# Kernel tuning notes

Hardware: AMD Instinct MI355X
Metric: run time of the kernel (lower is better)

## Reference

```python
import jax, jax.numpy as jnp
import numpy as np

B, T, C, H = 1, 1024, 2048, 32
N = C // H  # head_dim = 64
EPS_GN = 0.00064


def setup_inputs() -> dict:
    key = jax.random.key(0)
    ks = jax.random.split(key, 40)
    f32 = jnp.float32

    def rn(k, shape, s):
        return jax.random.normal(k, shape, f32) * s

    layer_idx, n_layer = 12, 24
    r01 = layer_idx / (n_layer - 1)
    r1a0 = 1.0 - layer_idx / n_layer
    ddd = (jnp.arange(C, dtype=f32) / C).reshape(1, 1, C)
    decay_speed = -7.0 + 5.0 * (jnp.arange(C, dtype=f32) / (C - 1)) ** (0.85 + r01 ** 0.5)

    inp = dict(
        hidden_states=jax.random.normal(ks[0], (B, T, C), f32),
        Wq=rn(ks[1], (C, C), 0.02), Wk=rn(ks[2], (C, C), 0.02),
        Wv=rn(ks[3], (C, C), 0.02), Wo=rn(ks[4], (C, C), 0.02),
        time_maa_x=1.0 - ddd ** (0.6 * r1a0 ** 0.9),
        time_maa_rg=rn(ks[5], (1, 1, C), 0.01),
        time_maa_wa=rn(ks[6], (1, 1, C), 0.01),
        time_maa_k=rn(ks[7], (1, 1, C), 0.01),
        time_maa_v=rn(ks[8], (1, 1, C), 0.01),
        time_maa_w1=rn(ks[9], (C, 4 * 32), 0.01),
        time_maa_w2=rn(ks[10], (4, 32, C), 0.01),
        time_decay=decay_speed.reshape(1, 1, C) + 0.5,
        time_decay_w1=rn(ks[11], (C, 64), 0.01),
        time_decay_w2=rn(ks[12], (64, C), 0.01),
        time_aaaaa=rn(ks[13], (1, 1, C), 0.01),
        time_aaa_w1=rn(ks[14], (C, 16), 0.01),
        time_aaa_w2=rn(ks[15], (16, C), 0.01),
        time_kkk_w1=rn(ks[16], (C, 16), 0.01),
        time_kkk_w2=rn(ks[17], (16, C), 0.01),
        gate_w1=rn(ks[18], (C, 128), 0.01),
        gate_w2=rn(ks[19], (128, C), 0.01),
        time_misc_a=rn(ks[20], (1, 1, C), 0.01),
        ma_w1=rn(ks[21], (C, 16), 0.01),
        ma_w2=rn(ks[22], (16, C), 0.01),
        time_misc_k=rn(ks[23], (1, 1, C), 0.01),
        mk_w1=rn(ks[24], (C, 16), 0.01),
        mk_w2=rn(ks[25], (16, C), 0.01),
        time_faaaa=rn(ks[26], (1, 1, H, N), 0.01),
        ln_w=1.0 + rn(ks[27], (C,), 0.01),
        ln_b=rn(ks[28], (C,), 0.01),
    )
    return inp


def _wkv7(r, w, k, v, a, b):
    """RWKV7 matrix-state recurrence. Inputs [B,T,C]; per head state [N,N].
    state_t = state * exp(w_t) (per key-col) + (state @ a_t) b_t^T + v_t k_t^T;
    out_t = state_t @ r_t."""
    hs = lambda x: x.reshape(B, T, H, N)
    r, k, v, a, b = map(hs, (r, k, v, a, b))
    dec = jnp.exp(hs(w))  # w <= -0.5, decay in (0,1)

    def step(state, inp):
        r_t, d_t, k_t, v_t, a_t, b_t = inp  # each [B,H,N]
        sa = jnp.einsum('bhij,bhj->bhi', state, a_t)
        state = (state * d_t[:, :, None, :]
                 + sa[..., None] * b_t[:, :, None, :]
                 + v_t[..., None] * k_t[:, :, None, :])
        out = jnp.einsum('bhij,bhj->bhi', state, r_t)
        return state, out

    xs = tuple(jnp.moveaxis(t, 1, 0) for t in (r, dec, k, v, a, b))  # [T,B,H,N]
    state0 = jnp.zeros((B, H, N, N), r.dtype)
    _, out = jax.lax.scan(step, state0, xs)
    return jnp.moveaxis(out, 0, 1).reshape(B, T, C)


def _group_norm(x, w, b):
    xg = x.reshape(B, T, H, N)
    mu = xg.mean(-1, keepdims=True)
    var = xg.var(-1, keepdims=True)
    xn = (xg - mu) * jax.lax.rsqrt(var + EPS_GN)
    return xn.reshape(B, T, C) * w + b


def reference(hidden_states, Wq, Wk, Wv, Wo, time_maa_x, time_maa_rg, time_maa_wa,
              time_maa_k, time_maa_v, time_maa_w1, time_maa_w2, time_decay,
              time_decay_w1, time_decay_w2, time_aaaaa, time_aaa_w1, time_aaa_w2,
              time_kkk_w1, time_kkk_w2, gate_w1, gate_w2, time_misc_a, ma_w1, ma_w2,
              time_misc_k, mk_w1, mk_w2, time_faaaa, ln_w, ln_b):
    x = hidden_states  # T already multiple of 16, so no padding branch
    dxprev = jnp.pad(x, ((0, 0), (1, 0), (0, 0)))[:, :-1] - x  # token shift
    xxx = x + dxprev * time_maa_x
    mix = jnp.tanh(xxx @ time_maa_w1).reshape(B, T, 4, 32)
    mix = jnp.einsum('btfd,fdc->fbtc', mix, time_maa_w2)  # [4,B,T,C]
    mrg, mwa, mk_mix, mv = mix[0], mix[1], mix[2], mix[3]
    xrg = x + dxprev * (time_maa_rg + mrg)
    xwa = x + dxprev * (time_maa_wa + mwa)
    xk = x + dxprev * (time_maa_k + mk_mix)
    xv = x + dxprev * (time_maa_v + mv)

    r = xrg @ Wq
    w = -jax.nn.softplus(-(time_decay + jnp.tanh(xwa @ time_decay_w1) @ time_decay_w2)) - 0.5
    k = xk @ Wk
    v = xv @ Wv
    g = jnp.tanh(xrg @ gate_w1) @ gate_w2

    kk = k + jnp.tanh(xk @ time_kkk_w1) @ time_kkk_w2
    kkh = kk.reshape(B, T, H, N)
    kk = (kkh / jnp.maximum(jnp.linalg.norm(kkh, axis=-1, keepdims=True), 1e-12)).reshape(B, T, C)

    a = jax.nn.sigmoid(time_aaaaa + (xwa @ time_aaa_w1) @ time_aaa_w2)
    ma = jax.nn.sigmoid(time_misc_a + (xwa @ ma_w1) @ ma_w2)
    k = k * ma + k * a * (1.0 - ma)
    mk_g = jax.nn.sigmoid(time_misc_k + (xk @ mk_w1) @ mk_w2)
    k = k * jnp.exp(jnp.minimum(w * mk_g, 0.0))

    y = _wkv7(r, w, k, v, -kk, kk * a)
    y = _group_norm(y, ln_w, ln_b)
    rh, kh, vh = (t.reshape(B, T, H, N) for t in (r, k, v))
    y = y + ((rh * kh * time_faaaa).sum(-1, keepdims=True) * vh).reshape(B, T, C)
    return (y * g) @ Wo
```

## Files before the change

### kernel.cpp

```cpp
#include <hip/hip_runtime.h>


#define T_ 1024
#define C_ 2048
#define H_ 32
#define N_ 64

using half8  = __attribute__((ext_vector_type(8))) _Float16;
using half4  = __attribute__((ext_vector_type(4))) _Float16;
using floatx4 = __attribute__((ext_vector_type(4))) float;

#define DPP_ADD(v, ctrl) \
    ((v) + __int_as_float(__builtin_amdgcn_update_dpp( \
        0, __float_as_int(v), (ctrl), 0xf, 0xf, true)))
#define REDUCE16(v) do { \
    v = DPP_ADD(v, 0xB1); v = DPP_ADD(v, 0x4E); \
    v = DPP_ADD(v, 0x141); v = DPP_ADD(v, 0x140); } while (0)

__device__ __forceinline__ void async_cp16(const void* g, void* l) {
    __builtin_amdgcn_global_load_lds(
        (const __attribute__((address_space(1))) void*)g,
        (__attribute__((address_space(3))) void*)l, 16, 0, 0);
}

__global__ __launch_bounds__(256) void k_tr(
    const float* __restrict__ W0, const float* __restrict__ W1,
    const float* __restrict__ W2, const float* __restrict__ W3,
    _Float16* __restrict__ D0, _Float16* __restrict__ D1,
    _Float16* __restrict__ D2, _Float16* __restrict__ D3)
{
    const int z = blockIdx.z;
    const float* S = (z == 0) ? W0 : (z == 1) ? W1 : (z == 2) ? W2 : W3;
    _Float16* D = (z == 0) ? D0 : (z == 1) ? D1 : (z == 2) ? D2 : D3;
    const int nb = blockIdx.x * 64, kb = blockIdx.y * 64;
    __shared__ __align__(16) float tile[64][65];
    const int tr = threadIdx.x >> 4, tc4 = (threadIdx.x & 15) * 4;
#pragma unroll
    for (int p = 0; p < 4; ++p) {
        int row = p * 16 + tr;
        float4 v = *(const float4*)&S[(size_t)(kb + row) * C_ + nb + tc4];
        tile[row][tc4 + 0] = v.x; tile[row][tc4 + 1] = v.y;
        tile[row][tc4 + 2] = v.z; tile[row][tc4 + 3] = v.w;
    }
    __syncthreads();
#pragma unroll
    for (int p = 0; p < 4; ++p) {
        int n = p * 16 + tr;
        half4 u;
        u[0] = (_Float16)tile[tc4 + 0][n];
        u[1] = (_Float16)tile[tc4 + 1][n];
        u[2] = (_Float16)tile[tc4 + 2][n];
        u[3] = (_Float16)tile[tc4 + 3][n];
        *(half4*)&D[(size_t)(nb + n) * C_ + kb + tc4] = u;
    }
}

__global__ __launch_bounds__(256) void k_trW(
    const float* __restrict__ maa_w1, const float* __restrict__ gate_w1,
    const float* __restrict__ decay_w1, const float* __restrict__ aaa_w1,
    const float* __restrict__ ma_w1, const float* __restrict__ kkk_w1,
    const float* __restrict__ mk_w1,
    _Float16* __restrict__ WTm, _Float16* __restrict__ WTl)
{
    const int z = blockIdx.z;
    const int k = blockIdx.x * 256 + threadIdx.x;
    const int n = blockIdx.y;
    if (z == 0 && n >= 128) return;
    const float* src; int stride, col;
    _Float16* dst;
    if (z == 0) { src = maa_w1; stride = 128; col = n; dst = WTm; }
    else {
        dst = WTl;
        if (n < 128)      { src = gate_w1;  stride = 128; col = n; }
        else if (n < 192) { src = decay_w1; stride = 64;  col = n - 128; }
        else if (n < 208) { src = aaa_w1;   stride = 16;  col = n - 192; }
        else if (n < 224) { src = ma_w1;    stride = 16;  col = n - 208; }
        else if (n < 240) { src = kkk_w1;   stride = 16;  col = n - 224; }
        else              { src = mk_w1;    stride = 16;  col = n - 240; }
    }
    dst[(size_t)n * C_ + k] = (_Float16)src[(size_t)k * stride + col];
}

__global__ __launch_bounds__(256) void k_prep(
    const float* __restrict__ X, const float* __restrict__ maa_x,
    _Float16* __restrict__ xxxH)
{
    const size_t idx = (size_t)blockIdx.x * 256 + threadIdx.x;
    const int c = (int)(idx & (C_ - 1));
    float cur = X[idx];
    float prev = (idx >= C_) ? X[idx - C_] : 0.0f;
    xxxH[idx] = (_Float16)(cur + (prev - cur) * maa_x[c]);
}

__global__ __launch_bounds__(256) void k_lora(
    int which,
    const _Float16* __restrict__ Axxx, const _Float16* __restrict__ Axrg,
    const _Float16* __restrict__ Axwa, const _Float16* __restrict__ Axk,
    const _Float16* __restrict__ WTm, const _Float16* __restrict__ WTl,
    float* __restrict__ m1p, float* __restrict__ l2p)
{
    const int mt = blockIdx.x;
    const int nt = blockIdx.y;
    const int ks = blockIdx.z;
    const _Float16* A; const _Float16* BT; float* O; int ostride;
    if (which == 0) { A = Axxx; BT = WTm; O = m1p; ostride = 128; }
    else {
        BT = WTl; O = l2p; ostride = 256;
        A = (nt < 4) ? Axrg : (nt < 7) ? Axwa : Axk;
    }
    O += (size_t)ks * T_ * ostride;
    const int m0 = mt * 64, n0 = nt * 32, k0 = ks * 512;
    const int tid = threadIdx.x;
    __shared__ __align__(16) _Float16 As[64 * 40];
    __shared__ __align__(16) _Float16 Bs[32 * 40];
    const int lane = tid & 63, wv = tid >> 6;
    const int r16 = lane & 15, q = lane >> 4;

    floatx4 acc[2];
    { floatx4 zv = {0.f, 0.f, 0.f, 0.f}; acc[0] = zv; acc[1] = zv; }

    const int arow = tid >> 2, ac8 = (tid & 3) * 8;
    const _Float16* ag = A + (size_t)(m0 + arow) * C_ + k0 + ac8;
    const _Float16* bg = BT + (size_t)(n0 + (tid >> 2)) * C_ + k0 + ac8;

    for (int kc = 0; kc < 512; kc += 32) {
        half8 av = *(const half8*)(ag + kc);
        half8 bv;
        if (tid < 128) bv = *(const half8*)(bg + kc);
        *(half8*)&As[arow * 40 + ac8] = av;
        if (tid < 128) *(half8*)&Bs[(tid >> 2) * 40 + ac8] = bv;
        __syncthreads();
        half8 af = *(const half8*)&As[(wv * 16 + r16) * 40 + q * 8];
        half8 b0 = *(const half8*)&Bs[(r16) * 40 + q * 8];
        half8 b1 = *(const half8*)&Bs[(16 + r16) * 40 + q * 8];
        acc[0] = __builtin_amdgcn_mfma_f32_16x16x32_f16(af, b0, acc[0], 0, 0, 0);
        acc[1] = __builtin_amdgcn_mfma_f32_16x16x32_f16(af, b1, acc[1], 0, 0, 0);
        __syncthreads();
    }
#pragma unroll
    for (int j = 0; j < 2; ++j)
#pragma unroll
        for (int e = 0; e < 4; ++e) {
            int row = m0 + wv * 16 + q * 4 + e;
            int col = n0 + j * 16 + r16;
            O[(size_t)row * ostride + col] = acc[j][e];
        }
}

__global__ __launch_bounds__(256) void k_xmix(
    const float* __restrict__ X, const float* __restrict__ m1p,
    const float* __restrict__ w2,
    const float* __restrict__ mrg, const float* __restrict__ mwa,
    const float* __restrict__ mk, const float* __restrict__ mv,
    _Float16* __restrict__ xrgH, _Float16* __restrict__ xwaH,
    _Float16* __restrict__ xkH, _Float16* __restrict__ xvH)
{
    const int tid = threadIdx.x;
    const int c = blockIdx.x * 256 + tid;
    const int t0 = blockIdx.y * 16;
    const size_t P = (size_t)T_ * 128;
    __shared__ __align__(16) float m1s[16][128];
#pragma unroll
    for (int p = 0; p < 2; ++p) {
        int id = tid + p * 256;
        int r = id >> 5, c4 = (id & 31) * 4;
        size_t off = (size_t)(t0 + r) * 128 + c4;
        float4 v0 = *(const float4*)&m1p[off];
        float4 v1 = *(const float4*)&m1p[P + off];
        float4 v2 = *(const float4*)&m1p[2 * P + off];
        float4 v3 = *(const float4*)&m1p[3 * P + off];
        float4 v;
        v.x = tanhf(((v0.x + v1.x) + v2.x) + v3.x);
        v.y = tanhf(((v0.y + v1.y) + v2.y) + v3.y);
        v.z = tanhf(((v0.z + v1.z) + v2.z) + v3.z);
        v.w = tanhf(((v0.w + v1.w) + v2.w) + v3.w);
        *(float4*)&m1s[r][c4] = v;
    }
    __syncthreads();
    float a0[16], a1[16], a2[16], a3[16];
#pragma unroll
    for (int t = 0; t < 16; ++t) { a0[t] = 0.f; a1[t] = 0.f; a2[t] = 0.f; a3[t] = 0.f; }
    for (int d = 0; d < 32; ++d) {
        float w0 = w2[(size_t)(0 * 32 + d) * C_ + c];
        float w1 = w2[(size_t)(1 * 32 + d) * C_ + c];
        float w2v = w2[(size_t)(2 * 32 + d) * C_ + c];
        float w3 = w2[(size_t)(3 * 32 + d) * C_ + c];
#pragma unroll
        for (int t = 0; t < 16; ++t) {
            a0[t] = fmaf(m1s[t][d],      w0,  a0[t]);
            a1[t] = fmaf(m1s[t][32 + d], w1,  a1[t]);
            a2[t] = fmaf(m1s[t][64 + d], w2v, a2[t]);
            a3[t] = fmaf(m1s[t][96 + d], w3,  a3[t]);
        }
    }
    float vrg = mrg[c], vwa = mwa[c], vmk = mk[c], vmv = mv[c];
    float prev = (t0 > 0) ? X[(size_t)(t0 - 1) * C_ + c] : 0.0f;
    for (int t = 0; t < 16; ++t) {
        size_t idx = (size_t)(t0 + t) * C_ + c;
        float cur = X[idx];
        float dx = prev - cur;
        xrgH[idx] = (_Float16)(cur + dx * (vrg + a0[t]));
        xwaH[idx] = (_Float16)(cur + dx * (vwa + a1[t]));
        xkH[idx]  = (_Float16)(cur + dx * (vmk + a2[t]));
        xvH[idx]  = (_Float16)(cur + dx * (vmv + a3[t]));
        prev = cur;
    }
}

__global__ __launch_bounds__(256) void k_gemm(
    const _Float16* __restrict__ A0, const _Float16* __restrict__ B0, float* __restrict__ C0,
    const _Float16* __restrict__ A1, const _Float16* __restrict__ B1, float* __restrict__ C1,
    const _Float16* __restrict__ A2, const _Float16* __restrict__ B2, float* __restrict__ C2)
{
    const int z = blockIdx.z;
    const _Float16* A = (z == 0) ? A0 : (z == 1) ? A1 : A2;
    const _Float16* Bt = (z == 0) ? B0 : (z == 1) ? B1 : B2;
    float* C = (z == 0) ? C0 : (z == 1) ? C1 : C2;
    const int mtile = blockIdx.y * 128;
    const int ntile = blockIdx.x * 128;
    const int tid = threadIdx.x;
    __shared__ __align__(16) _Float16 As[3][128 * 32];
    __shared__ __align__(16) _Float16 Bs[3][128 * 32];
    const int lane = tid & 63;
    const int wvid = tid >> 6;
    const int wm = wvid >> 1, wn = wvid & 1;
    const int r16 = lane & 15, q = lane >> 4;
    const int qs = (q ^ ((r16 >> 1) & 3)) * 8;

    floatx4 acc[4][4];
#pragma unroll
    for (int i = 0; i < 4; ++i)
#pragma unroll
        for (int j = 0; j < 4; ++j) { floatx4 zv = {0.f, 0.f, 0.f, 0.f}; acc[i][j] = zv; }

    const int srow = tid >> 2, sq = tid & 3;
    const int sqg = (sq ^ ((srow >> 1) & 3)) * 8;
    const _Float16* agA = A + (size_t)(mtile + srow) * C_ + sqg;
    const _Float16* agB = Bt + (size_t)(ntile + srow) * C_ + sqg;
    const int ldso = srow * 32 + sq * 8;
    const size_t rowoff = (size_t)64 * C_;

#define G_STAGE(pb, koff) do {                                                \
        async_cp16(agA + (koff), &As[pb][ldso]);                              \
        async_cp16(agA + (koff) + rowoff, &As[pb][ldso + 64 * 32]);           \
        async_cp16(agB + (koff), &Bs[pb][ldso]);                              \
        async_cp16(agB + (koff) + rowoff, &Bs[pb][ldso + 64 * 32]);           \
    } while (0)

    G_STAGE(0, 0);
    G_STAGE(1, 32);
    __builtin_amdgcn_sched_barrier(0);
    asm volatile("s_waitcnt vmcnt(4)" ::: "memory");
    __builtin_amdgcn_s_barrier();
    __builtin_amdgcn_sched_barrier(0);

    for (int ks = 0; ks < 64; ++ks) {
        const int p = ks % 3;
        if (ks + 2 < 64) G_STAGE((ks + 2) % 3, (ks + 2) * 32);
        half8 af[4], bf[4];
#pragma unroll
        for (int i = 0; i < 4; ++i)
            af[i] = *(const half8*)&As[p][(wm * 64 + i * 16 + r16) * 32 + qs];
#pragma unroll
        for (int j = 0; j < 4; ++j)
            bf[j] = *(const half8*)&Bs[p][(wn * 64 + j * 16 + r16) * 32 + qs];
#pragma unroll
        for (int i = 0; i < 4; ++i)
#pragma unroll
            for (int j = 0; j < 4; ++j)
                acc[i][j] = __builtin_amdgcn_mfma_f32_16x16x32_f16(af[i], bf[j], acc[i][j], 0, 0, 0);
        __builtin_amdgcn_sched_barrier(0);
        if (ks + 2 < 64)
            asm volatile("s_waitcnt vmcnt(4)" ::: "memory");
        else
            asm volatile("s_waitcnt vmcnt(0)" ::: "memory");
        __builtin_amdgcn_s_barrier();
        __builtin_amdgcn_sched_barrier(0);
    }
#pragma unroll
    for (int i = 0; i < 4; ++i)
#pragma unroll
        for (int j = 0; j < 4; ++j)
#pragma unroll
            for (int e = 0; e < 4; ++e) {
                int row = mtile + wm * 64 + i * 16 + q * 4 + e;
                int col = ntile + wn * 64 + j * 16 + r16;
                C[(size_t)row * C_ + col] = acc[i][j][e];
            }
#undef G_STAGE
}

__global__ __launch_bounds__(256) void k_gemm64(
    const _Float16* __restrict__ A0, const _Float16* __restrict__ B0, float* __restrict__ C0)
{
    const _Float16* A = A0;
    const _Float16* Bt = B0;
    float* C = C0;
    const int mtile = blockIdx.y * 128;
    const int ntile = blockIdx.x * 64;
    const int tid = threadIdx.x;
    __shared__ __align__(16) _Float16 As[3][128 * 32];
    __shared__ __align__(16) _Float16 Bs[3][64 * 32];
    const int lane = tid & 63;
    const int wvid = tid >> 6;
    const int wm = wvid >> 1, wn = wvid & 1;
    const int r16 = lane & 15, q = lane >> 4;
    const int qs = (q ^ ((r16 >> 1) & 3)) * 8;

    floatx4 acc[4][2];
#pragma unroll
    for (int i = 0; i < 4; ++i)
#pragma unroll
        for (int j = 0; j < 2; ++j) { floatx4 zv = {0.f, 0.f, 0.f, 0.f}; acc[i][j] = zv; }

    const int srow = tid >> 2, sq = tid & 3;
    const int sqg = (sq ^ ((srow >> 1) & 3)) * 8;
    const _Float16* agA = A + (size_t)(mtile + srow) * C_ + sqg;
    const _Float16* agB = Bt + (size_t)(ntile + srow) * C_ + sqg;
    const int ldso = srow * 32 + sq * 8;
    const size_t rowoff = (size_t)64 * C_;

#define G_STAGE(pb, koff) do {                                                \
        async_cp16(agA + (koff), &As[pb][ldso]);                              \
        async_cp16(agA + (koff) + rowoff, &As[pb][ldso + 64 * 32]);           \
        async_cp16(agB + (koff), &Bs[pb][ldso]);                              \
    } while (0)

    G_STAGE(0, 0);
    G_STAGE(1, 32);
    __builtin_amdgcn_sched_barrier(0);
    asm volatile("s_waitcnt vmcnt(3)" ::: "memory");
    __builtin_amdgcn_s_barrier();
    __builtin_amdgcn_sched_barrier(0);

    for (int ks = 0; ks < 64; ++ks) {
        const int p = ks % 3;
        if (ks + 2 < 64) G_STAGE((ks + 2) % 3, (ks + 2) * 32);
        half8 af[4], bf[2];
#pragma unroll
        for (int i = 0; i < 4; ++i)
            af[i] = *(const half8*)&As[p][(wm * 64 + i * 16 + r16) * 32 + qs];
#pragma unroll
        for (int j = 0; j < 2; ++j)
            bf[j] = *(const half8*)&Bs[p][(wn * 32 + j * 16 + r16) * 32 + qs];
#pragma unroll
        for (int i = 0; i < 4; ++i)
#pragma unroll
            for (int j = 0; j < 2; ++j)
                acc[i][j] = __builtin_amdgcn_mfma_f32_16x16x32_f16(af[i], bf[j], acc[i][j], 0, 0, 0);
        __builtin_amdgcn_sched_barrier(0);
        if (ks + 2 < 64)
            asm volatile("s_waitcnt vmcnt(3)" ::: "memory");
        else
            asm volatile("s_waitcnt vmcnt(0)" ::: "memory");
        __builtin_amdgcn_s_barrier();
        __builtin_amdgcn_sched_barrier(0);
    }
#pragma unroll
    for (int i = 0; i < 4; ++i)
#pragma unroll
        for (int j = 0; j < 2; ++j)
#pragma unroll
            for (int e = 0; e < 4; ++e) {
                int row = mtile + wm * 64 + i * 16 + q * 4 + e;
                int col = ntile + wn * 32 + j * 16 + r16;
                C[(size_t)row * C_ + col] = acc[i][j][e];
            }
#undef G_STAGE
}

__global__ __launch_bounds__(256) void k_fuse(
    const float* __restrict__ l2p,
    float* __restrict__ K0,
    const float* __restrict__ decay_w2, const float* __restrict__ aaa_w2,
    const float* __restrict__ ma_w2, const float* __restrict__ kkk_w2,
    const float* __restrict__ mk_w2,
    const float* __restrict__ tdecay, const float* __restrict__ aaaaa,
    const float* __restrict__ misc_a, const float* __restrict__ misc_k,
    float* __restrict__ Dout, float* __restrict__ KKout, float* __restrict__ Bout)
{
    const int tid = threadIdx.x;
    const int c = blockIdx.x * 256 + tid;
    const int t0 = blockIdx.y * 4;
    const size_t P = (size_t)T_ * 256;
    __shared__ __align__(16) float wsS[4][96];
    __shared__ __align__(16) float ksS[4][32];
    if (tid < 4 * 24) {
        int r = tid / 24, c4 = (tid % 24) * 4;
        size_t off = (size_t)(t0 + r) * 256 + 128 + c4;
        float4 v0 = *(const float4*)&l2p[off];
        float4 v1 = *(const float4*)&l2p[P + off];
        float4 v2 = *(const float4*)&l2p[2 * P + off];
        float4 v3 = *(const float4*)&l2p[3 * P + off];
        float4 v;
        v.x = ((v0.x + v1.x) + v2.x) + v3.x;
        v.y = ((v0.y + v1.y) + v2.y) + v3.y;
        v.z = ((v0.z + v1.z) + v2.z) + v3.z;
        v.w = ((v0.w + v1.w) + v2.w) + v3.w;
        if (c4 < 64) { v.x = tanhf(v.x); v.y = tanhf(v.y); v.z = tanhf(v.z); v.w = tanhf(v.w); }
        *(float4*)&wsS[r][c4] = v;
    }
    if (tid < 4 * 8) {
        int r = tid / 8, c4 = (tid % 8) * 4;
        size_t off = (size_t)(t0 + r) * 256 + 224 + c4;
        float4 v0 = *(const float4*)&l2p[off];
        float4 v1 = *(const float4*)&l2p[P + off];
        float4 v2 = *(const float4*)&l2p[2 * P + off];
        float4 v3 = *(const float4*)&l2p[3 * P + off];
        float4 v;
        v.x = ((v0.x + v1.x) + v2.x) + v3.x;
        v.y = ((v0.y + v1.y) + v2.y) + v3.y;
        v.z = ((v0.z + v1.z) + v2.z) + v3.z;
        v.w = ((v0.w + v1.w) + v2.w) + v3.w;
        if (c4 < 16) { v.x = tanhf(v.x); v.y = tanhf(v.y); v.z = tanhf(v.z); v.w = tanhf(v.w); }
        *(float4*)&ksS[r][c4] = v;
    }
    __syncthreads();
    float accW[4], accA[4], accMA[4], accKK[4], accMK[4];
#pragma unroll
    for (int r = 0; r < 4; ++r) { accW[r] = 0.f; accA[r] = 0.f; accMA[r] = 0.f; accKK[r] = 0.f; accMK[r] = 0.f; }
    for (int j = 0; j < 64; ++j) {
        float w = decay_w2[(size_t)j * C_ + c];
#pragma unroll
        for (int r = 0; r < 4; ++r) accW[r] = fmaf(wsS[r][j], w, accW[r]);
    }
    for (int j = 0; j < 16; ++j) {
        float wa = aaa_w2[(size_t)j * C_ + c];
        float wm = ma_w2[(size_t)j * C_ + c];
        float wk = kkk_w2[(size_t)j * C_ + c];
        float wq = mk_w2[(size_t)j * C_ + c];
#pragma unroll
        for (int r = 0; r < 4; ++r) {
            accA[r]  = fmaf(wsS[r][64 + j], wa, accA[r]);
            accMA[r] = fmaf(wsS[r][80 + j], wm, accMA[r]);
            accKK[r] = fmaf(ksS[r][j],      wk, accKK[r]);
            accMK[r] = fmaf(ksS[r][16 + j], wq, accMK[r]);
        }
    }
    float td = tdecay[c], aa = aaaaa[c], mia = misc_a[c], mik = misc_k[c];
#pragma unroll
    for (int r = 0; r < 4; ++r) {
        size_t idx = (size_t)(t0 + r) * C_ + c;
        float wraw = td + accW[r];
        float w = -__logf(1.0f + __expf(-wraw)) - 0.5f;
        float a  = 1.0f / (1.0f + __expf(-(aa  + accA[r])));
        float mav = 1.0f / (1.0f + __expf(-(mia + accMA[r])));
        float mkv = 1.0f / (1.0f + __expf(-(mik + accMK[r])));
        float k0 = K0[idx];
        float kkun = k0 + accKK[r];
        float ss = kkun * kkun;
        REDUCE16(ss);
        ss += __shfl_xor(ss, 16, 64);
        ss += __shfl_xor(ss, 32, 64);
        float kn = kkun * (1.0f / fmaxf(sqrtf(ss), 1e-12f));
        Dout[idx]  = __expf(w);
        KKout[idx] = kn;
        Bout[idx]  = kn * a;
        K0[idx]    = k0 * (mav + a * (1.0f - mav)) * __expf(fminf(w * mkv, 0.0f));
    }
}

__global__ __launch_bounds__(512) void k_wkv_p1(
    const float* __restrict__ DEC, const float* __restrict__ K,
    const float* __restrict__ V, const float* __restrict__ KK,
    const float* __restrict__ Bb,
    float* __restrict__ Send, float* __restrict__ Pend)
{
    const int tid = threadIdx.x;
    const int g = blockIdx.x;
    const int h = blockIdx.y;
    const int c0 = h * 64;
    const int wv = tid >> 6, lane = tid & 63;
    const int jg = lane & 15, q = lane >> 4, j4 = jg * 4;
    const bool isS = wv < 4;
    const int row0 = (isS ? wv : wv - 4) * 16 + q * 4;

    __shared__ __align__(16) float dS[2][16][64], kS[2][16][64], vS[2][16][64],
                                   aS[2][16][64], bS[2][16][64];

    const int pos = tid & 255, grp = tid >> 8;
    const int pst = pos >> 4, pq4 = (pos & 15) * 4;

#define P1_STAGE(buf, tcb) do {                                               \
    size_t gg = (size_t)((tcb) + pst) * C_ + c0 + pq4;                        \
    if (grp == 0) { async_cp16(&DEC[gg], &dS[buf][pst][pq4]);                 \
                    async_cp16(&KK[gg],  &aS[buf][pst][pq4]);                 \
                    async_cp16(&Bb[gg],  &bS[buf][pst][pq4]); }               \
    else          { async_cp16(&K[gg], &kS[buf][pst][pq4]);                   \
                    async_cp16(&V[gg], &vS[buf][pst][pq4]); }                 \
} while (0)

    float4 s0, s1, s2, s3;
    if (isS) {
        s0 = make_float4(0.f, 0.f, 0.f, 0.f); s1 = s0; s2 = s0; s3 = s0;
    } else {
#define IDROW(m) make_float4((j4 + 0 == row0 + (m)) ? 1.f : 0.f,              \
                             (j4 + 1 == row0 + (m)) ? 1.f : 0.f,              \
                             (j4 + 2 == row0 + (m)) ? 1.f : 0.f,              \
                             (j4 + 3 == row0 + (m)) ? 1.f : 0.f)
        s0 = IDROW(0); s1 = IDROW(1); s2 = IDROW(2); s3 = IDROW(3);
#undef IDROW
    }

    const int t0 = g * 64;
    P1_STAGE(0, t0);

    for (int tc = 0; tc < 64; tc += 16) {
        const int p = (tc >> 4) & 1;
        __syncthreads();
        if (tc + 16 < 64) P1_STAGE(p ^ 1, t0 + tc + 16);
#pragma unroll
        for (int tt = 0; tt < 16; ++tt) {
            float4 cd = *(float4*)&dS[p][tt][j4];
            float4 ca = *(float4*)&aS[p][tt][j4];
            float4 cb = *(float4*)&bS[p][tt][j4];
            float4 ck, vv;
            if (isS) {
                ck = *(float4*)&kS[p][tt][j4];
                vv = *(float4*)&vS[p][tt][row0];
            } else {
                ck = make_float4(0.f, 0.f, 0.f, 0.f);
                vv = make_float4(0.f, 0.f, 0.f, 0.f);
            }
            float sa0 = -(fmaf(s0.y, ca.y, s0.x * ca.x) + fmaf(s0.w, ca.w, s0.z * ca.z));
            float sa1 = -(fmaf(s1.y, ca.y, s1.x * ca.x) + fmaf(s1.w, ca.w, s1.z * ca.z));
            float sa2 = -(fmaf(s2.y, ca.y, s2.x * ca.x) + fmaf(s2.w, ca.w, s2.z * ca.z));
            float sa3 = -(fmaf(s3.y, ca.y, s3.x * ca.x) + fmaf(s3.w, ca.w, s3.z * ca.z));
            REDUCE16(sa0); REDUCE16(sa1); REDUCE16(sa2); REDUCE16(sa3);
            s0.x = fmaf(s0.x, cd.x, fmaf(sa0, cb.x, vv.x * ck.x));
            s0.y = fmaf(s0.y, cd.y, fmaf(sa0, cb.y, vv.x * ck.y));
            s0.z = fmaf(s0.z, cd.z, fmaf(sa0, cb.z, vv.x * ck.z));
            s0.w = fmaf(s0.w, cd.w, fmaf(sa0, cb.w, vv.x * ck.w));
            s1.x = fmaf(s1.x, cd.x, fmaf(sa1, cb.x, vv.y * ck.x));
            s1.y = fmaf(s1.y, cd.y, fmaf(sa1, cb.y, vv.y * ck.y));
            s1.z = fmaf(s1.z, cd.z, fmaf(sa1, cb.z, vv.y * ck.z));
            s1.w = fmaf(s1.w, cd.w, fmaf(sa1, cb.w, vv.y * ck.w));
            s2.x = fmaf(s2.x, cd.x, fmaf(sa2, cb.x, vv.z * ck.x));
            s2.y = fmaf(s2.y, cd.y, fmaf(sa2, cb.y, vv.z * ck.y));
            s2.z = fmaf(s2.z, cd.z, fmaf(sa2, cb.z, vv.z * ck.z));
            s2.w = fmaf(s2.w, cd.w, fmaf(sa2, cb.w, vv.z * ck.w));
            s3.x = fmaf(s3.x, cd.x, fmaf(sa3, cb.x, vv.w * ck.x));
            s3.y = fmaf(s3.y, cd.y, fmaf(sa3, cb.y, vv.w * ck.y));
            s3.z = fmaf(s3.z, cd.z, fmaf(sa3, cb.z, vv.w * ck.z));
            s3.w = fmaf(s3.w, cd.w, fmaf(sa3, cb.w, vv.w * ck.w));
        }
    }
    float* dst = isS ? Send : Pend;
    size_t base = (size_t)((h * 15 + g) * 64 + row0) * 64 + j4;
    *(float4*)&dst[base +   0] = s0;
    *(float4*)&dst[base +  64] = s1;
    *(float4*)&dst[base + 128] = s2;
    *(float4*)&dst[base + 192] = s3;
#undef P1_STAGE
}

__global__ __launch_bounds__(1024) void k_wkv_comb(
    const float* __restrict__ Send, const float* __restrict__ Pend,
    float* __restrict__ Sin)
{
    const int h = blockIdx.x;
    const int tid = threadIdx.x;
    const int i = tid >> 4;
    const int jq = (tid & 15) * 4;
    __shared__ float Sc[64][65];
    __shared__ __align__(16) float Pl[64][64];

    float4 z4 = make_float4(0.f, 0.f, 0.f, 0.f);
    *(float4*)&Sin[(size_t)(h * 16) * 4096 + (size_t)i * 64 + jq] = z4;
    Sc[i][jq + 0] = 0.f; Sc[i][jq + 1] = 0.f;
    Sc[i][jq + 2] = 0.f; Sc[i][jq + 3] = 0.f;
    __syncthreads();

    for (int g = 1; g < 16; ++g) {
        const float* Pg = &Pend[(size_t)(h * 15 + g - 1) * 4096];
        {
            int idx = tid * 4;
            float4 v = *(const float4*)&Pg[idx];
            *(float4*)&Pl[idx >> 6][idx & 63] = v;
        }
        __syncthreads();
        float acc[4];
        {
            float4 sv = *(const float4*)&Send[
                (size_t)(h * 15 + g - 1) * 4096 + (size_t)i * 64 + jq];
            acc[0] = sv.x; acc[1] = sv.y; acc[2] = sv.z; acc[3] = sv.w;
        }
        for (int k = 0; k < 64; ++k) {
            float sik = Sc[i][k];
#pragma unroll
            for (int c = 0; c < 4; ++c) acc[c] = fmaf(sik, Pl[k][jq + c], acc[c]);
        }
        __syncthreads();
        float* So = &Sin[(size_t)(h * 16 + g) * 4096 + (size_t)i * 64 + jq];
        Sc[i][jq + 0] = acc[0]; Sc[i][jq + 1] = acc[1];
        Sc[i][jq + 2] = acc[2]; Sc[i][jq + 3] = acc[3];
        *(float4*)So = make_float4(acc[0], acc[1], acc[2], acc[3]);
        __syncthreads();
    }
}

__global__ __launch_bounds__(256) void k_wkv_p2(
    const float* __restrict__ R, const float* __restrict__ DEC,
    const float* __restrict__ K, const float* __restrict__ V,
    const float* __restrict__ KK, const float* __restrict__ Bb,
    const float* __restrict__ Sin, float* __restrict__ Y)
{
    const int tid = threadIdx.x;
    const int g = blockIdx.x;
    const int h = blockIdx.y;
    const int c0 = h * 64;
    const int wv = tid >> 6, lane = tid & 63;
    const int jg = lane & 15, q = lane >> 4, j4 = jg * 4;
    const int row0 = wv * 16 + q * 4;

    __shared__ __align__(16) float rS[2][16][64], dS[2][16][64], kS[2][16][64],
                                   aS[2][16][64], bS[2][16][64], vS[2][16][64];

    const int pst = tid >> 4, pq4 = (tid & 15) * 4;

#define P2_STAGE(buf, tcb) do {                                               \
    size_t gg = (size_t)((tcb) + pst) * C_ + c0 + pq4;                        \
    async_cp16(&R[gg],   &rS[buf][pst][pq4]);                                 \
    async_cp16(&DEC[gg], &dS[buf][pst][pq4]);                                 \
    async_cp16(&K[gg],   &kS[buf][pst][pq4]);                                 \
    async_cp16(&V[gg],   &vS[buf][pst][pq4]);                                 \
    async_cp16(&KK[gg],  &aS[buf][pst][pq4]);                                 \
    async_cp16(&Bb[gg],  &bS[buf][pst][pq4]);                                 \
} while (0)

    float4 s0, s1, s2, s3;
    {
        const float* Sb = &Sin[(size_t)((h * 16 + g) * 64 + row0) * 64 + j4];
        s0 = *(const float4*)&Sb[0];
        s1 = *(const float4*)&Sb[64];
        s2 = *(const float4*)&Sb[128];
        s3 = *(const float4*)&Sb[192];
    }

    const int t0 = g * 64;
    P2_STAGE(0, t0);

    for (int tc = 0; tc < 64; tc += 16) {
        const int p = (tc >> 4) & 1;
        __syncthreads();
        if (tc + 16 < 64) P2_STAGE(p ^ 1, t0 + tc + 16);
#pragma unroll
        for (int hh = 0; hh < 2; ++hh) {
            float po0[8], po1[8], po2[8], po3[8];
#pragma unroll
            for (int qs2 = 0; qs2 < 8; ++qs2) {
                const int tt = hh * 8 + qs2;
                float4 cr = *(float4*)&rS[p][tt][j4];
                float4 cd = *(float4*)&dS[p][tt][j4];
                float4 ck = *(float4*)&kS[p][tt][j4];
                float4 ca = *(float4*)&aS[p][tt][j4];
                float4 cb = *(float4*)&bS[p][tt][j4];
                float4 vv = *(float4*)&vS[p][tt][row0];
                float sa0 = -(fmaf(s0.y, ca.y, s0.x * ca.x) + fmaf(s0.w, ca.w, s0.z * ca.z));
                float sa1 = -(fmaf(s1.y, ca.y, s1.x * ca.x) + fmaf(s1.w, ca.w, s1.z * ca.z));
                float sa2 = -(fmaf(s2.y, ca.y, s2.x * ca.x) + fmaf(s2.w, ca.w, s2.z * ca.z));
                float sa3 = -(fmaf(s3.y, ca.y, s3.x * ca.x) + fmaf(s3.w, ca.w, s3.z * ca.z));
                REDUCE16(sa0); REDUCE16(sa1); REDUCE16(sa2); REDUCE16(sa3);
                s0.x = fmaf(s0.x, cd.x, fmaf(sa0, cb.x, vv.x * ck.x));
                s0.y = fmaf(s0.y, cd.y, fmaf(sa0, cb.y, vv.x * ck.y));
                s0.z = fmaf(s0.z, cd.z, fmaf(sa0, cb.z, vv.x * ck.z));
                s0.w = fmaf(s0.w, cd.w, fmaf(sa0, cb.w, vv.x * ck.w));
                s1.x = fmaf(s1.x, cd.x, fmaf(sa1, cb.x, vv.y * ck.x));
                s1.y = fmaf(s1.y, cd.y, fmaf(sa1, cb.y, vv.y * ck.y));
                s1.z = fmaf(s1.z, cd.z, fmaf(sa1, cb.z, vv.y * ck.z));
                s1.w = fmaf(s1.w, cd.w, fmaf(sa1, cb.w, vv.y * ck.w));
                s2.x = fmaf(s2.x, cd.x, fmaf(sa2, cb.x, vv.z * ck.x));
                s2.y = fmaf(s2.y, cd.y, fmaf(sa2, cb.y, vv.z * ck.y));
                s2.z = fmaf(s2.z, cd.z, fmaf(sa2, cb.z, vv.z * ck.z));
                s2.w = fmaf(s2.w, cd.w, fmaf(sa2, cb.w, vv.z * ck.w));
                s3.x = fmaf(s3.x, cd.x, fmaf(sa3, cb.x, vv.w * ck.x));
                s3.y = fmaf(s3.y, cd.y, fmaf(sa3, cb.y, vv.w * ck.y));
                s3.z = fmaf(s3.z, cd.z, fmaf(sa3, cb.z, vv.w * ck.z));
                s3.w = fmaf(s3.w, cd.w, fmaf(sa3, cb.w, vv.w * ck.w));
                po0[qs2] = fmaf(s0.w, cr.w, fmaf(s0.z, cr.z, fmaf(s0.y, cr.y, s0.x * cr.x)));
                po1[qs2] = fmaf(s1.w, cr.w, fmaf(s1.z, cr.z, fmaf(s1.y, cr.y, s1.x * cr.x)));
                po2[qs2] = fmaf(s2.w, cr.w, fmaf(s2.z, cr.z, fmaf(s2.y, cr.y, s2.x * cr.x)));
                po3[qs2] = fmaf(s3.w, cr.w, fmaf(s3.z, cr.z, fmaf(s3.y, cr.y, s3.x * cr.x)));
            }
#pragma unroll
            for (int qs2 = 0; qs2 < 8; ++qs2) {
                REDUCE16(po0[qs2]); REDUCE16(po1[qs2]);
                REDUCE16(po2[qs2]); REDUCE16(po3[qs2]);
            }
            if (jg == 0) {
#pragma unroll
                for (int qs2 = 0; qs2 < 8; ++qs2) {
                    float4 o = make_float4(po0[qs2], po1[qs2], po2[qs2], po3[qs2]);
                    *(float4*)&Y[(size_t)(t0 + tc + hh * 8 + qs2) * C_ + c0 + row0] = o;
                }
            }
        }
    }
#undef P2_STAGE
}

__global__ __launch_bounds__(256) void k_gn(
    const float* __restrict__ Y, const float* __restrict__ R, const float* __restrict__ K,
    const float* __restrict__ V, const float* __restrict__ l2p,
    const float* __restrict__ gw2,
    const float* __restrict__ faaaa, const float* __restrict__ lnw,
    const float* __restrict__ lnb, _Float16* __restrict__ YG)
{
    const int tid = threadIdx.x;
    const int c = blockIdx.x * 256 + tid;
    const int t0 = blockIdx.y * 16;
    const size_t P = (size_t)T_ * 256;
    __shared__ __align__(16) float gs[16][128];
    for (int id = tid; id < 16 * 128; id += 256) {
        int r = id >> 7, cc = id & 127;
        size_t off = (size_t)(t0 + r) * 256 + cc;
        float v = ((l2p[off] + l2p[P + off]) + l2p[2 * P + off]) + l2p[3 * P + off];
        gs[r][cc] = tanhf(v);
    }
    __syncthreads();
    float gacc[16];
#pragma unroll
    for (int r = 0; r < 16; ++r) gacc[r] = 0.f;
    for (int j = 0; j < 128; ++j) {
        float w = gw2[(size_t)j * C_ + c];
#pragma unroll
        for (int r = 0; r < 16; ++r) gacc[r] = fmaf(gs[r][j], w, gacc[r]);
    }
    float fa = faaaa[c], lw = lnw[c], lb = lnb[c];
    for (int r = 0; r < 16; ++r) {
        const size_t idx = (size_t)(t0 + r) * C_ + c;
        float y = Y[idx];
        float s1 = y, s2 = y * y;
#pragma unroll
        for (int off = 1; off < 64; off <<= 1) {
            s1 += __shfl_xor(s1, off, 64);
            s2 += __shfl_xor(s2, off, 64);
        }
        float mu = s1 * (1.0f / 64.0f);
        float var = s2 * (1.0f / 64.0f) - mu * mu;
        float gn = (y - mu) * rsqrtf(var + 0.00064f) * lw + lb;
        float p = R[idx] * K[idx] * fa;
#pragma unroll
        for (int off = 1; off < 64; off <<= 1) p += __shfl_xor(p, off, 64);
        float y2 = gn + p * V[idx];
        YG[idx] = (_Float16)(y2 * gacc[r]);
    }
}

extern "C" void kernel_launch(void* const* d_in, const int* in_sizes, int n_in,
                              void* d_out, int out_size, void* d_ws, size_t ws_size,
                              hipStream_t stream)
{
    (void)in_sizes; (void)n_in; (void)out_size; (void)ws_size;
    const float* hidden   = (const float*)d_in[0];
    const float* Wq       = (const float*)d_in[1];
    const float* Wk       = (const float*)d_in[2];
    const float* Wv       = (const float*)d_in[3];
    const float* Wo       = (const float*)d_in[4];
    const float* maa_x    = (const float*)d_in[5];
    const float* maa_rg   = (const float*)d_in[6];
    const float* maa_wa   = (const float*)d_in[7];
    const float* maa_k    = (const float*)d_in[8];
    const float* maa_v    = (const float*)d_in[9];
    const float* maa_w1   = (const float*)d_in[10];
    const float* maa_w2   = (const float*)d_in[11];
    const float* tdecay   = (const float*)d_in[12];
    const float* decay_w1 = (const float*)d_in[13];
    const float* decay_w2 = (const float*)d_in[14];
    const float* aaaaa    = (const float*)d_in[15];
    const float* aaa_w1   = (const float*)d_in[16];
    const float* aaa_w2   = (const float*)d_in[17];
    const float* kkk_w1   = (const float*)d_in[18];
    const float* kkk_w2   = (const float*)d_in[19];
    const float* gate_w1  = (const float*)d_in[20];
    const float* gate_w2  = (const float*)d_in[21];
    const float* misc_a   = (const float*)d_in[22];
    const float* ma_w1    = (const float*)d_in[23];
    const float* ma_w2    = (const float*)d_in[24];
    const float* misc_k   = (const float*)d_in[25];
    const float* mk_w1    = (const float*)d_in[26];
    const float* mk_w2    = (const float*)d_in[27];
    const float* faaaa    = (const float*)d_in[28];
    const float* lnw      = (const float*)d_in[29];
    const float* lnb      = (const float*)d_in[30];

    float* ws = (float*)d_ws;
    const size_t TC = (size_t)T_ * C_;
    float* S0 = ws + 0 * TC;
    float* Send = ws + 1 * TC;
    float* S2 = ws + 2 * TC;
    float* S3 = ws + 3 * TC;
    float* S4 = ws + 4 * TC;
    float* S5 = ws + 5 * TC;
    float* S6 = ws + 6 * TC;
    float* S7 = ws + 7 * TC;
    float* m1p = ws + 8 * TC;
    float* l2p = m1p + (size_t)4 * T_ * 128;
    _Float16* WTq = (_Float16*)(l2p + (size_t)4 * T_ * 256);
    _Float16* WTk = WTq + (size_t)C_ * C_;
    _Float16* WTv = WTk + (size_t)C_ * C_;
    _Float16* WTo = WTv + (size_t)C_ * C_;
    _Float16* WTm = WTo + (size_t)C_ * C_;
    _Float16* WTl = WTm + (size_t)128 * C_;
    _Float16* xxxH = WTl + (size_t)256 * C_;
    _Float16* xrgH = xxxH + TC;
    _Float16* xwaH = xrgH + TC;
    _Float16* xkH  = xwaH + TC;
    _Float16* xvH  = xkH + TC;
    _Float16* ygH  = xxxH;
    float* Sin  = (float*)xrgH;
    float* Pend = (float*)xkH;
    float* out = (float*)d_out;

    k_tr<<<dim3(32, 32, 4), 256, 0, stream>>>(Wq, Wk, Wv, Wo, WTq, WTk, WTv, WTo);
    k_trW<<<dim3(8, 256, 2), 256, 0, stream>>>(maa_w1, gate_w1, decay_w1,
        aaa_w1, ma_w1, kkk_w1, mk_w1, WTm, WTl);
    k_prep<<<dim3((int)(TC / 256)), 256, 0, stream>>>(hidden, maa_x, xxxH);
    k_lora<<<dim3(16, 4, 4), 256, 0, stream>>>(0, xxxH, xxxH, xxxH, xxxH,
        WTm, WTl, m1p, l2p);
    k_xmix<<<dim3(8, 64), 256, 0, stream>>>(hidden, m1p, maa_w2,
        maa_rg, maa_wa, maa_k, maa_v, xrgH, xwaH, xkH, xvH);
    k_lora<<<dim3(16, 8, 4), 256, 0, stream>>>(1, xxxH, xrgH, xwaH, xkH,
        WTm, WTl, m1p, l2p);
    k_gemm<<<dim3(16, 8, 3), 256, 0, stream>>>(
        xrgH, WTq, S4,  xkH, WTk, S6,  xvH, WTv, S7);
    k_fuse<<<dim3(8, 256), 256, 0, stream>>>(l2p, S6, decay_w2, aaa_w2, ma_w2,
        kkk_w2, mk_w2, tdecay, aaaaa, misc_a, misc_k, S5, S3, S2);
    k_wkv_p1<<<dim3(15, 32), 512, 0, stream>>>(S5, S6, S7, S3, S2, Send, Pend);
    k_wkv_comb<<<dim3(32), 1024, 0, stream>>>(Send, Pend, Sin);
    k_wkv_p2<<<dim3(16, 32), 256, 0, stream>>>(S4, S5, S6, S7, S3, S2, Sin, S0);
    k_gn<<<dim3(8, 64), 256, 0, stream>>>(S0, S4, S6, S7, l2p, gate_w2,
        faaaa, lnw, lnb, ygH);
    k_gemm64<<<dim3(32, 8, 1), 256, 0, stream>>>(ygH, WTo, out);
}
```

Measured before the change: 524.0 us.

## Fold prep into weight transpose, double-buffer LoRA, split-K output GEMM, prefetch combine

The token-shift prep kernel is merged into the weight-transpose launch as an extra z-slice, with float4 vectorisation. The LoRA GEMM gains double-buffered shared memory so the next K-chunk's global loads overlap the MFMAs, and one barrier per iteration is removed. The final output GEMM is split along K into two partial buffers, doubling the grid to fill more CUs, and a separate reduction kernel sums them. The WKV combine kernel prefetches the next chunk's P and S and drops one barrier per step. The costs are an extra launch, extra partial-sum traffic, and reuse of scratch buffers (S2, Sin) as partial outputs.

Result: faster. 512.4 us (-2.2%).

```diff
diff --git a/kernel.cpp b/kernel.cpp
--- a/kernel.cpp
+++ b/kernel.cpp
@@ -60,10 +60,28 @@
     const float* __restrict__ decay_w1, const float* __restrict__ aaa_w1,
     const float* __restrict__ ma_w1, const float* __restrict__ kkk_w1,
     const float* __restrict__ mk_w1,
-    _Float16* __restrict__ WTm, _Float16* __restrict__ WTl)
+    const float* __restrict__ X, const float* __restrict__ maa_x,
+    _Float16* __restrict__ WTm, _Float16* __restrict__ WTl,
+    _Float16* __restrict__ xxxH)
 {
     const int z = blockIdx.z;
-    const int k = blockIdx.x * 256 + threadIdx.x;
+    const int tid = threadIdx.x;
+    if (z == 2) {
+        const size_t e0 = ((size_t)(blockIdx.y * 8 + blockIdx.x) * 256 + tid) * 4;
+        float4 cur = *(const float4*)&X[e0];
+        float4 prev = make_float4(0.f, 0.f, 0.f, 0.f);
+        if (e0 >= C_) prev = *(const float4*)&X[e0 - C_];
+        const int c = (int)(e0 & (C_ - 1));
+        float4 mx = *(const float4*)&maa_x[c];
+        half4 o;
+        o[0] = (_Float16)(cur.x + (prev.x - cur.x) * mx.x);
+        o[1] = (_Float16)(cur.y + (prev.y - cur.y) * mx.y);
+        o[2] = (_Float16)(cur.z + (prev.z - cur.z) * mx.z);
+        o[3] = (_Float16)(cur.w + (prev.w - cur.w) * mx.w);
+        *(half4*)&xxxH[e0] = o;
+        return;
+    }
+    const int k = blockIdx.x * 256 + tid;
     const int n = blockIdx.y;
     if (z == 0 && n >= 128) return;
     const float* src; int stride, col;
@@ -81,17 +99,6 @@
     dst[(size_t)n * C_ + k] = (_Float16)src[(size_t)k * stride + col];
 }
 
-__global__ __launch_bounds__(256) void k_prep(
-    const float* __restrict__ X, const float* __restrict__ maa_x,
-    _Float16* __restrict__ xxxH)
-{
-    const size_t idx = (size_t)blockIdx.x * 256 + threadIdx.x;
-    const int c = (int)(idx & (C_ - 1));
-    float cur = X[idx];
-    float prev = (idx >= C_) ? X[idx - C_] : 0.0f;
-    xxxH[idx] = (_Float16)(cur + (prev - cur) * maa_x[c]);
-}
-
 __global__ __launch_bounds__(256) void k_lora(
     int which,
     const _Float16* __restrict__ Axxx, const _Float16* __restrict__ Axrg,
@@ -111,8 +118,8 @@
     O += (size_t)ks * T_ * ostride;
     const int m0 = mt * 64, n0 = nt * 32, k0 = ks * 512;
     const int tid = threadIdx.x;
-    __shared__ __align__(16) _Float16 As[64 * 40];
-    __shared__ __align__(16) _Float16 Bs[32 * 40];
+    __shared__ __align__(16) _Float16 As[2][64 * 40];
+    __shared__ __align__(16) _Float16 Bs[2][32 * 40];
     const int lane = tid & 63, wv = tid >> 6;
     const int r16 = lane & 15, q = lane >> 4;
 
@@ -121,20 +128,34 @@
 
     const int arow = tid >> 2, ac8 = (tid & 3) * 8;
     const _Float16* ag = A + (size_t)(m0 + arow) * C_ + k0 + ac8;
-    const _Float16* bg = BT + (size_t)(n0 + (tid >> 2)) * C_ + k0 + ac8;
-
-    for (int kc = 0; kc < 512; kc += 32) {
-        half8 av = *(const half8*)(ag + kc);
-        half8 bv;
-        if (tid < 128) bv = *(const half8*)(bg + kc);
-        *(half8*)&As[arow * 40 + ac8] = av;
-        if (tid < 128) *(half8*)&Bs[(tid >> 2) * 40 + ac8] = bv;
-        __syncthreads();
-        half8 af = *(const half8*)&As[(wv * 16 + r16) * 40 + q * 8];
-        half8 b0 = *(const half8*)&Bs[(r16) * 40 + q * 8];
-        half8 b1 = *(const half8*)&Bs[(16 + r16) * 40 + q * 8];
+    const _Float16* bg = BT + (size_t)(n0 + arow) * C_ + k0 + ac8;
+
+    {
+        half8 av = *(const half8*)ag;
+        *(half8*)&As[0][arow * 40 + ac8] = av;
+        if (tid < 128) {
+            half8 bv = *(const half8*)bg;
+            *(half8*)&Bs[0][arow * 40 + ac8] = bv;
+        }
+    }
+    __syncthreads();
+
+    for (int it = 0; it < 16; ++it) {
+        const int p = it & 1;
+        half8 av2, bv2;
+        if (it < 15) {
+            av2 = *(const half8*)(ag + (it + 1) * 32);
+            if (tid < 128) bv2 = *(const half8*)(bg + (it + 1) * 32);
+        }
+        half8 af = *(const half8*)&As[p][(wv * 16 + r16) * 40 + q * 8];
+        half8 b0 = *(const half8*)&Bs[p][(r16) * 40 + q * 8];
+        half8 b1 = *(const half8*)&Bs[p][(16 + r16) * 40 + q * 8];
         acc[0] = __builtin_amdgcn_mfma_f32_16x16x32_f16(af, b0, acc[0], 0, 0, 0);
         acc[1] = __builtin_amdgcn_mfma_f32_16x16x32_f16(af, b1, acc[1], 0, 0, 0);
+        if (it < 15) {
+            *(half8*)&As[p ^ 1][arow * 40 + ac8] = av2;
+            if (tid < 128) *(half8*)&Bs[p ^ 1][arow * 40 + ac8] = bv2;
+        }
         __syncthreads();
     }
 #pragma unroll
@@ -291,11 +312,13 @@
 }
 
 __global__ __launch_bounds__(256) void k_gemm64(
-    const _Float16* __restrict__ A0, const _Float16* __restrict__ B0, float* __restrict__ C0)
+    const _Float16* __restrict__ A0, const _Float16* __restrict__ B0,
+    float* __restrict__ P0, float* __restrict__ P1)
 {
     const _Float16* A = A0;
     const _Float16* Bt = B0;
-    float* C = C0;
+    float* C = (blockIdx.z == 0) ? P0 : P1;
+    const int k0 = blockIdx.z * 1024;
     const int mtile = blockIdx.y * 128;
     const int ntile = blockIdx.x * 64;
     const int tid = threadIdx.x;
@@ -315,8 +338,8 @@
 
     const int srow = tid >> 2, sq = tid & 3;
     const int sqg = (sq ^ ((srow >> 1) & 3)) * 8;
-    const _Float16* agA = A + (size_t)(mtile + srow) * C_ + sqg;
-    const _Float16* agB = Bt + (size_t)(ntile + srow) * C_ + sqg;
+    const _Float16* agA = A + (size_t)(mtile + srow) * C_ + k0 + sqg;
+    const _Float16* agB = Bt + (size_t)(ntile + srow) * C_ + k0 + sqg;
     const int ldso = srow * 32 + sq * 8;
     const size_t rowoff = (size_t)64 * C_;
 
@@ -333,9 +356,9 @@
     __builtin_amdgcn_s_barrier();
     __builtin_amdgcn_sched_barrier(0);
 
-    for (int ks = 0; ks < 64; ++ks) {
+    for (int ks = 0; ks < 32; ++ks) {
         const int p = ks % 3;
-        if (ks + 2 < 64) G_STAGE((ks + 2) % 3, (ks + 2) * 32);
+        if (ks + 2 < 32) G_STAGE((ks + 2) % 3, (ks + 2) * 32);
         half8 af[4], bf[2];
 #pragma unroll
         for (int i = 0; i < 4; ++i)
@@ -349,7 +372,7 @@
             for (int j = 0; j < 2; ++j)
                 acc[i][j] = __builtin_amdgcn_mfma_f32_16x16x32_f16(af[i], bf[j], acc[i][j], 0, 0, 0);
         __builtin_amdgcn_sched_barrier(0);
-        if (ks + 2 < 64)
+        if (ks + 2 < 32)
             asm volatile("s_waitcnt vmcnt(3)" ::: "memory");
         else
             asm volatile("s_waitcnt vmcnt(0)" ::: "memory");
@@ -367,6 +390,18 @@
                 C[(size_t)row * C_ + col] = acc[i][j][e];
             }
 #undef G_STAGE
+}
+
+__global__ __launch_bounds__(256) void k_red(
+    const float* __restrict__ P0, const float* __restrict__ P1,
+    float* __restrict__ O)
+{
+    const size_t i = ((size_t)blockIdx.x * 256 + threadIdx.x) * 4;
+    float4 a = *(const float4*)&P0[i];
+    float4 b = *(const float4*)&P1[i];
+    float4 o;
+    o.x = a.x + b.x; o.y = a.y + b.y; o.z = a.z + b.z; o.w = a.w + b.w;
+    *(float4*)&O[i] = o;
 }
 
 __global__ __launch_bounds__(256) void k_fuse(
@@ -562,6 +597,7 @@
     const int tid = threadIdx.x;
     const int i = tid >> 4;
     const int jq = (tid & 15) * 4;
+    const int idx = tid * 4;
     __shared__ float Sc[64][65];
     __shared__ __align__(16) float Pl[64][64];
 
@@ -569,33 +605,30 @@
     *(float4*)&Sin[(size_t)(h * 16) * 4096 + (size_t)i * 64 + jq] = z4;
     Sc[i][jq + 0] = 0.f; Sc[i][jq + 1] = 0.f;
     Sc[i][jq + 2] = 0.f; Sc[i][jq + 3] = 0.f;
+    float4 pv = *(const float4*)&Pend[(size_t)(h * 15) * 4096 + idx];
+    float4 sv = *(const float4*)&Send[(size_t)(h * 15) * 4096 + (size_t)i * 64 + jq];
     __syncthreads();
 
     for (int g = 1; g < 16; ++g) {
-        const float* Pg = &Pend[(size_t)(h * 15 + g - 1) * 4096];
-        {
-            int idx = tid * 4;
-            float4 v = *(const float4*)&Pg[idx];
-            *(float4*)&Pl[idx >> 6][idx & 63] = v;
-        }
+        *(float4*)&Pl[idx >> 6][idx & 63] = pv;
         __syncthreads();
-        float acc[4];
-        {
-            float4 sv = *(const float4*)&Send[
-                (size_t)(h * 15 + g - 1) * 4096 + (size_t)i * 64 + jq];
-            acc[0] = sv.x; acc[1] = sv.y; acc[2] = sv.z; acc[3] = sv.w;
-        }
+        float4 pv2 = z4, sv2 = z4;
+        if (g < 15) {
+            pv2 = *(const float4*)&Pend[(size_t)(h * 15 + g) * 4096 + idx];
+            sv2 = *(const float4*)&Send[(size_t)(h * 15 + g) * 4096 + (size_t)i * 64 + jq];
+        }
+        float acc[4] = {sv.x, sv.y, sv.z, sv.w};
         for (int k = 0; k < 64; ++k) {
             float sik = Sc[i][k];
 #pragma unroll
             for (int c = 0; c < 4; ++c) acc[c] = fmaf(sik, Pl[k][jq + c], acc[c]);
         }
         __syncthreads();
-        float* So = &Sin[(size_t)(h * 16 + g) * 4096 + (size_t)i * 64 + jq];
         Sc[i][jq + 0] = acc[0]; Sc[i][jq + 1] = acc[1];
         Sc[i][jq + 2] = acc[2]; Sc[i][jq + 3] = acc[3];
-        *(float4*)So = make_float4(acc[0], acc[1], acc[2], acc[3]);
-        __syncthreads();
+        *(float4*)&Sin[(size_t)(h * 16 + g) * 4096 + (size_t)i * 64 + jq] =
+            make_float4(acc[0], acc[1], acc[2], acc[3]);
+        pv = pv2; sv = sv2;
     }
 }
 
@@ -810,12 +843,13 @@
     _Float16* ygH  = xxxH;
     float* Sin  = (float*)xrgH;
     float* Pend = (float*)xkH;
+    float* GP0 = S2;
+    float* GP1 = Sin;
     float* out = (float*)d_out;
 
     k_tr<<<dim3(32, 32, 4), 256, 0, stream>>>(Wq, Wk, Wv, Wo, WTq, WTk, WTv, WTo);
-    k_trW<<<dim3(8, 256, 2), 256, 0, stream>>>(maa_w1, gate_w1, decay_w1,
-        aaa_w1, ma_w1, kkk_w1, mk_w1, WTm, WTl);
-    k_prep<<<dim3((int)(TC / 256)), 256, 0, stream>>>(hidden, maa_x, xxxH);
+    k_trW<<<dim3(8, 256, 3), 256, 0, stream>>>(maa_w1, gate_w1, decay_w1,
+        aaa_w1, ma_w1, kkk_w1, mk_w1, hidden, maa_x, WTm, WTl, xxxH);
     k_lora<<<dim3(16, 4, 4), 256, 0, stream>>>(0, xxxH, xxxH, xxxH, xxxH,
         WTm, WTl, m1p, l2p);
     k_xmix<<<dim3(8, 64), 256, 0, stream>>>(hidden, m1p, maa_w2,
@@ -831,5 +865,6 @@
     k_wkv_p2<<<dim3(16, 32), 256, 0, stream>>>(S4, S5, S6, S7, S3, S2, Sin, S0);
     k_gn<<<dim3(8, 64), 256, 0, stream>>>(S0, S4, S6, S7, l2p, gate_w2,
         faaaa, lnw, lnb, ygH);
-    k_gemm64<<<dim3(32, 8, 1), 256, 0, stream>>>(ygH, WTo, out);
-}
+    k_gemm64<<<dim3(32, 8, 2), 256, 0, stream>>>(ygH, WTo, GP0, GP1);
+    k_red<<<dim3(2048), 256, 0, stream>>>(GP0, GP1, out);
+}
```
